# Kernel optimization log

Measured on AMD Instinct MI355X. Metric: run time of the kernel, lower is better.

## Reference

```python
import jax, jax.numpy as jnp
import numpy as np

B, S, D = 32, 512, 768
EPS = 1e-8  # torch CosineSimilarity eps

def setup_inputs() -> dict:
    key = jax.random.key(0)
    k1, k2, k3, k4 = jax.random.split(key, 4)
    emb1 = jax.random.normal(k1, (B, S, D), jnp.float32)
    emb2 = jax.random.normal(k2, (B, S, D), jnp.float32)
    mask1 = jax.random.randint(k3, (B, S), 0, 2).astype(jnp.int32)
    mask2 = jax.random.randint(k4, (B, S), 0, 2).astype(jnp.int32)
    return {"emb1": emb1, "emb2": emb2, "mask1": mask1, "mask2": mask2}

def reference(emb1, emb2, mask1, mask2):
    # normalize token embeddings (cosine sim = dot of unit vectors)
    n1 = emb1 / jnp.maximum(jnp.linalg.norm(emb1, axis=-1, keepdims=True), EPS)
    n2 = emb2 / jnp.maximum(jnp.linalg.norm(emb2, axis=-1, keepdims=True), EPS)
    # full pairwise cosine similarity: [B, S1, S2]
    sim = jnp.einsum('bid,bjd->bij', n1, n2)
    m1 = mask1.astype(sim.dtype)
    m2 = mask2.astype(sim.dtype)
    valid = m1[:, :, None] * m2[:, None, :]
    neg_inf = jnp.asarray(-jnp.inf, sim.dtype)
    masked = jnp.where(valid > 0, sim, neg_inf)
    # row max over valid cols; rows with no valid token contribute 0
    row_max = jnp.where(m1 > 0, jnp.max(masked, axis=2), 0.0)  # [B, S1]
    col_max = jnp.where(m2 > 0, jnp.max(masked, axis=1), 0.0)  # [B, S2]
    denom = jnp.sum(m1, axis=1) + jnp.sum(m2, axis=1)          # n1 + n2
    score = (jnp.sum(row_max, axis=1) + jnp.sum(col_max, axis=1)) / jnp.maximum(denom, 1.0)
    return score  # [B]
```

## Files before the change

### kernel.cpp

```cpp
#include <hip/hip_runtime.h>

#define BB 32
#define SS 512
#define DD 768

typedef float f32x4 __attribute__((ext_vector_type(4)));
typedef short bf16x8 __attribute__((ext_vector_type(8)));

__device__ __forceinline__ unsigned fkey(float f) {
  unsigned u = __float_as_uint(f);
  return (u & 0x80000000u) ? ~u : (u | 0x80000000u);
}
__device__ __forceinline__ float fdecode(unsigned k) {
  return __uint_as_float((k & 0x80000000u) ? (k & 0x7fffffffu) : ~k);
}
__device__ __forceinline__ unsigned short cvt_bf16(float f) {
  unsigned u = __float_as_uint(f);
  u += 0x7fffu + ((u >> 16) & 1u);
  return (unsigned short)(u >> 16);
}

__global__ __launch_bounds__(256) void norms_kernel(
    const float* __restrict__ emb1, const float* __restrict__ emb2,
    float* __restrict__ inv1, float* __restrict__ inv2,
    unsigned* __restrict__ rowkey, unsigned* __restrict__ colkey) {
  int wave = blockIdx.x * 4 + (threadIdx.x >> 6);
  int lane = threadIdx.x & 63;
  int half = wave >> 14;
  int r = wave & 16383;
  const float* src = (half ? emb2 : emb1) + (size_t)r * DD;
  const float4* p = (const float4*)src;
  float s = 0.f;
#pragma unroll
  for (int q = 0; q < 3; ++q) {
    float4 v = p[q * 64 + lane];
    s += v.x * v.x + v.y * v.y + v.z * v.z + v.w * v.w;
  }
#pragma unroll
  for (int m = 1; m < 64; m <<= 1) s += __shfl_xor(s, m);
  if (lane == 0) {
    float inv = 1.0f / fmaxf(sqrtf(s), 1e-8f);
    if (half == 0) { inv1[r] = inv; rowkey[r] = 0x007fffffu; }
    else           { inv2[r] = inv; colkey[r] = 0x007fffffu; }
  }
}

__global__ __launch_bounds__(256) void simmax_kernel(
    const float* __restrict__ emb1, const float* __restrict__ emb2,
    const int* __restrict__ mask1, const int* __restrict__ mask2,
    const float* __restrict__ inv1, const float* __restrict__ inv2,
    unsigned* __restrict__ rowkey, unsigned* __restrict__ colkey) {
  int b = blockIdx.y;
  int i0 = (blockIdx.x >> 2) << 7;
  int j0 = (blockIdx.x & 3) << 7;
  __shared__ __align__(16) unsigned short sA[128 * 64];
  __shared__ __align__(16) unsigned short sB[128 * 64];
  __shared__ float sInv1[128], sInv2[128];
  __shared__ int sM1[128], sM2[128];
  int t = threadIdx.x;
  if (t < 128) {
    sInv1[t] = inv1[b * SS + i0 + t];
    sM1[t]   = mask1[b * SS + i0 + t];
  } else {
    int u = t - 128;
    sInv2[u] = inv2[b * SS + j0 + u];
    sM2[u]   = mask2[b * SS + j0 + u];
  }
  const float* Ab = emb1 + ((size_t)b * SS + i0) * DD;
  const float* Bb = emb2 + ((size_t)b * SS + j0) * DD;
  int l = t & 63, wid = t >> 6, wr = wid >> 1, wc = wid & 1;
  f32x4 acc[4][4] = {};

  for (int k0 = 0; k0 < DD; k0 += 64) {
    __syncthreads();
#pragma unroll 4
    for (int pp = 0; pp < 8; ++pp) {
      int flat = pp * 256 + t;
      int r = flat >> 4, f4 = flat & 15;
      const float4 va = *(const float4*)(Ab + (size_t)r * DD + k0 + f4 * 4);
      const float4 vb = *(const float4*)(Bb + (size_t)r * DD + k0 + f4 * 4);
      int el = (r << 6) + ((((f4 >> 1) ^ (r & 7)) << 3) | ((f4 & 1) << 2));
      ushort4 ua, ub;
      ua.x = cvt_bf16(va.x); ua.y = cvt_bf16(va.y); ua.z = cvt_bf16(va.z); ua.w = cvt_bf16(va.w);
      ub.x = cvt_bf16(vb.x); ub.y = cvt_bf16(vb.y); ub.z = cvt_bf16(vb.z); ub.w = cvt_bf16(vb.w);
      *(ushort4*)(&sA[el]) = ua;
      *(ushort4*)(&sB[el]) = ub;
    }
    __syncthreads();
#pragma unroll
    for (int kk = 0; kk < 2; ++kk) {
      bf16x8 af[4], bfr[4];
#pragma unroll
      for (int mi = 0; mi < 4; ++mi) {
        int r = wr * 64 + mi * 16 + (l & 15);
        int ch = (kk << 2) + (l >> 4);
        af[mi] = *(const bf16x8*)(&sA[(r << 6) + ((ch ^ (r & 7)) << 3)]);
      }
#pragma unroll
      for (int ni = 0; ni < 4; ++ni) {
        int r = wc * 64 + ni * 16 + (l & 15);
        int ch = (kk << 2) + (l >> 4);
        bfr[ni] = *(const bf16x8*)(&sB[(r << 6) + ((ch ^ (r & 7)) << 3)]);
      }
#pragma unroll
      for (int mi = 0; mi < 4; ++mi)
#pragma unroll
        for (int ni = 0; ni < 4; ++ni)
          acc[mi][ni] = __builtin_amdgcn_mfma_f32_16x16x32_bf16(af[mi], bfr[ni], acc[mi][ni], 0, 0, 0);
    }
  }

  const float NEG = -__builtin_inff();
  float rmax[4][4], cmax[4];
#pragma unroll
  for (int mi = 0; mi < 4; ++mi)
#pragma unroll
    for (int rg = 0; rg < 4; ++rg) rmax[mi][rg] = NEG;
#pragma unroll
  for (int ni = 0; ni < 4; ++ni) cmax[ni] = NEG;

#pragma unroll
  for (int mi = 0; mi < 4; ++mi) {
#pragma unroll
    for (int ni = 0; ni < 4; ++ni) {
#pragma unroll
      for (int rg = 0; rg < 4; ++rg) {
        int rl = wr * 64 + mi * 16 + (l >> 4) * 4 + rg;
        int cl = wc * 64 + ni * 16 + (l & 15);
        float v = acc[mi][ni][rg] * sInv1[rl] * sInv2[cl];
        v = (sM1[rl] && sM2[cl]) ? v : NEG;
        rmax[mi][rg] = fmaxf(rmax[mi][rg], v);
        cmax[ni] = fmaxf(cmax[ni], v);
      }
    }
  }
#pragma unroll
  for (int mi = 0; mi < 4; ++mi)
#pragma unroll
    for (int rg = 0; rg < 4; ++rg) {
      float v = rmax[mi][rg];
      v = fmaxf(v, __shfl_xor(v, 1));
      v = fmaxf(v, __shfl_xor(v, 2));
      v = fmaxf(v, __shfl_xor(v, 4));
      v = fmaxf(v, __shfl_xor(v, 8));
      rmax[mi][rg] = v;
    }
#pragma unroll
  for (int ni = 0; ni < 4; ++ni) {
    float v = cmax[ni];
    v = fmaxf(v, __shfl_xor(v, 16));
    v = fmaxf(v, __shfl_xor(v, 32));
    cmax[ni] = v;
  }
  int selm = (l >> 2) & 3, selr = l & 3, seln = (l >> 4) & 3;
  float rv = rmax[0][0], cv = cmax[0];
#pragma unroll
  for (int mi = 0; mi < 4; ++mi)
#pragma unroll
    for (int rg = 0; rg < 4; ++rg)
      if (selm == mi && selr == rg) rv = rmax[mi][rg];
#pragma unroll
  for (int ni = 0; ni < 4; ++ni)
    if (seln == ni) cv = cmax[ni];
  int rl = selm * 16 + ((l >> 4) & 3) * 4 + selr;
  int cl = seln * 16 + (l & 15);
  atomicMax(&rowkey[b * SS + i0 + wr * 64 + rl], fkey(rv));
  atomicMax(&colkey[b * SS + j0 + wc * 64 + cl], fkey(cv));
}

__global__ __launch_bounds__(256) void finalize_kernel(
    const int* __restrict__ mask1, const int* __restrict__ mask2,
    const unsigned* __restrict__ rowkey, const unsigned* __restrict__ colkey,
    float* __restrict__ out) {
  int b = blockIdx.x, t = threadIdx.x;
  float sum = 0.f;
  int cnt = 0;
  for (int s = t; s < SS; s += 256) {
    if (mask1[b * SS + s]) { sum += fdecode(rowkey[b * SS + s]); cnt++; }
    if (mask2[b * SS + s]) { sum += fdecode(colkey[b * SS + s]); cnt++; }
  }
#pragma unroll
  for (int m = 1; m < 64; m <<= 1) {
    sum += __shfl_xor(sum, m);
    cnt += __shfl_xor(cnt, m);
  }
  __shared__ float sS[4];
  __shared__ int sC[4];
  int w = t >> 6, lane = t & 63;
  if (lane == 0) { sS[w] = sum; sC[w] = cnt; }
  __syncthreads();
  if (t == 0) {
    float T = sS[0] + sS[1] + sS[2] + sS[3];
    int C = sC[0] + sC[1] + sC[2] + sC[3];
    out[b] = T / fmaxf((float)C, 1.0f);
  }
}

extern "C" void kernel_launch(void* const* d_in, const int* in_sizes, int n_in,
                              void* d_out, int out_size, void* d_ws, size_t ws_size,
                              hipStream_t stream) {
  const float* emb1 = (const float*)d_in[0];
  const float* emb2 = (const float*)d_in[1];
  const int* mask1 = (const int*)d_in[2];
  const int* mask2 = (const int*)d_in[3];
  float* out = (float*)d_out;

  float* inv1 = (float*)d_ws;
  float* inv2 = inv1 + BB * SS;
  unsigned* rowkey = (unsigned*)(inv2 + BB * SS);
  unsigned* colkey = rowkey + BB * SS;

  norms_kernel<<<8192, 256, 0, stream>>>(emb1, emb2, inv1, inv2, rowkey, colkey);
  simmax_kernel<<<dim3(16, BB), 256, 0, stream>>>(emb1, emb2, mask1, mask2,
                                                  inv1, inv2, rowkey, colkey);
  finalize_kernel<<<BB, 256, 0, stream>>>(mask1, mask2, rowkey, colkey, out);
}
```

Baseline: 173.4 us.

## Pre-normalize to swizzled bf16 workspace and stream tiles via global_load_lds double buffering

The norm kernel now also scales each row by its inverse norm and writes it as bf16 in the swizzled shared-memory layout to a workspace. The matmul kernel then copies tiles straight into double-buffered LDS with global_load_lds, overlapping the next tile's load with MFMA work, and drops the per-element inverse-norm scaling. The 512 blocks are remapped so consecutive blocks cover different batches. This halves the bytes the matmul reads and removes in-loop conversion, at the cost of writing and rereading an extra bf16 workspace.

```diff
diff --git a/kernel.cpp b/kernel.cpp
--- a/kernel.cpp
+++ b/kernel.cpp
@@ -3,6 +3,7 @@
 #define BB 32
 #define SS 512
 #define DD 768
+#define NROW (BB * SS)
 
 typedef float f32x4 __attribute__((ext_vector_type(4)));
 typedef short bf16x8 __attribute__((ext_vector_type(8)));
@@ -20,73 +21,84 @@
   return (unsigned short)(u >> 16);
 }
 
-__global__ __launch_bounds__(256) void norms_kernel(
+__global__ __launch_bounds__(256) void norm_cvt_kernel(
     const float* __restrict__ emb1, const float* __restrict__ emb2,
-    float* __restrict__ inv1, float* __restrict__ inv2,
+    unsigned short* __restrict__ wsA, unsigned short* __restrict__ wsB,
     unsigned* __restrict__ rowkey, unsigned* __restrict__ colkey) {
   int wave = blockIdx.x * 4 + (threadIdx.x >> 6);
   int lane = threadIdx.x & 63;
   int half = wave >> 14;
-  int r = wave & 16383;
+  int r = wave & (NROW - 1);
   const float* src = (half ? emb2 : emb1) + (size_t)r * DD;
-  const float4* p = (const float4*)src;
+  float4 v[3];
   float s = 0.f;
 #pragma unroll
   for (int q = 0; q < 3; ++q) {
-    float4 v = p[q * 64 + lane];
-    s += v.x * v.x + v.y * v.y + v.z * v.z + v.w * v.w;
+    v[q] = ((const float4*)src)[q * 64 + lane];
+    s += v[q].x * v[q].x + v[q].y * v[q].y + v[q].z * v[q].z + v[q].w * v[q].w;
   }
 #pragma unroll
   for (int m = 1; m < 64; m <<= 1) s += __shfl_xor(s, m);
+  float inv = 1.0f / fmaxf(sqrtf(s), 1e-8f);
+  unsigned short* dst = (half ? wsB : wsA) + (size_t)r * DD;
+  int base = ((lane >> 4) << 6) + (((((lane >> 1) & 7) ^ (r & 7))) << 3) + ((lane & 1) << 2);
+#pragma unroll
+  for (int q = 0; q < 3; ++q) {
+    ushort4 u;
+    u.x = cvt_bf16(v[q].x * inv); u.y = cvt_bf16(v[q].y * inv);
+    u.z = cvt_bf16(v[q].z * inv); u.w = cvt_bf16(v[q].w * inv);
+    *(ushort4*)(dst + q * 256 + base) = u;
+  }
   if (lane == 0) {
-    float inv = 1.0f / fmaxf(sqrtf(s), 1e-8f);
-    if (half == 0) { inv1[r] = inv; rowkey[r] = 0x007fffffu; }
-    else           { inv2[r] = inv; colkey[r] = 0x007fffffu; }
+    if (half == 0) rowkey[r] = 0x007fffffu;
+    else           colkey[r] = 0x007fffffu;
   }
 }
 
 __global__ __launch_bounds__(256) void simmax_kernel(
-    const float* __restrict__ emb1, const float* __restrict__ emb2,
+    const unsigned short* __restrict__ wsA, const unsigned short* __restrict__ wsB,
     const int* __restrict__ mask1, const int* __restrict__ mask2,
-    const float* __restrict__ inv1, const float* __restrict__ inv2,
     unsigned* __restrict__ rowkey, unsigned* __restrict__ colkey) {
-  int b = blockIdx.y;
-  int i0 = (blockIdx.x >> 2) << 7;
-  int j0 = (blockIdx.x & 3) << 7;
-  __shared__ __align__(16) unsigned short sA[128 * 64];
-  __shared__ __align__(16) unsigned short sB[128 * 64];
-  __shared__ float sInv1[128], sInv2[128];
+  int x = blockIdx.x;
+  int b = (x & 7) + (((x >> 3) & 3) << 3);
+  int tile = x >> 5;
+  int i0 = (tile >> 2) << 7;
+  int j0 = (tile & 3) << 7;
+  __shared__ __align__(16) unsigned short sA[2][128 * 64];
+  __shared__ __align__(16) unsigned short sB[2][128 * 64];
   __shared__ int sM1[128], sM2[128];
-  int t = threadIdx.x;
-  if (t < 128) {
-    sInv1[t] = inv1[b * SS + i0 + t];
-    sM1[t]   = mask1[b * SS + i0 + t];
-  } else {
-    int u = t - 128;
-    sInv2[u] = inv2[b * SS + j0 + u];
-    sM2[u]   = mask2[b * SS + j0 + u];
-  }
-  const float* Ab = emb1 + ((size_t)b * SS + i0) * DD;
-  const float* Bb = emb2 + ((size_t)b * SS + j0) * DD;
-  int l = t & 63, wid = t >> 6, wr = wid >> 1, wc = wid & 1;
+  int t = threadIdx.x, l = t & 63, wid = t >> 6, wr = wid >> 1, wc = wid & 1;
+  if (t < 128) sM1[t] = mask1[b * SS + i0 + t];
+  else sM2[t - 128] = mask2[b * SS + j0 + (t - 128)];
+  const unsigned short* gA = wsA + (size_t)(b * SS + i0) * DD;
+  const unsigned short* gB = wsB + (size_t)(b * SS + j0) * DD;
+  int rsub = l >> 3, csub = l & 7;
+
   f32x4 acc[4][4] = {};
 
-  for (int k0 = 0; k0 < DD; k0 += 64) {
-    __syncthreads();
-#pragma unroll 4
-    for (int pp = 0; pp < 8; ++pp) {
-      int flat = pp * 256 + t;
-      int r = flat >> 4, f4 = flat & 15;
-      const float4 va = *(const float4*)(Ab + (size_t)r * DD + k0 + f4 * 4);
-      const float4 vb = *(const float4*)(Bb + (size_t)r * DD + k0 + f4 * 4);
-      int el = (r << 6) + ((((f4 >> 1) ^ (r & 7)) << 3) | ((f4 & 1) << 2));
-      ushort4 ua, ub;
-      ua.x = cvt_bf16(va.x); ua.y = cvt_bf16(va.y); ua.z = cvt_bf16(va.z); ua.w = cvt_bf16(va.w);
-      ub.x = cvt_bf16(vb.x); ub.y = cvt_bf16(vb.y); ub.z = cvt_bf16(vb.z); ub.w = cvt_bf16(vb.w);
-      *(ushort4*)(&sA[el]) = ua;
-      *(ushort4*)(&sB[el]) = ub;
-    }
-    __syncthreads();
+#define STAGE(buf, k0)                                                              \
+  {                                                                                 \
+    _Pragma("unroll") for (int j = 0; j < 4; ++j) {                                 \
+      int rowblk = (wid * 4 + j) * 8;                                               \
+      const unsigned short* ga = gA + (size_t)(rowblk + rsub) * DD + (k0) + csub * 8; \
+      const unsigned short* gb = gB + (size_t)(rowblk + rsub) * DD + (k0) + csub * 8; \
+      __builtin_amdgcn_global_load_lds(                                             \
+          (const __attribute__((address_space(1))) unsigned int*)ga,                \
+          (__attribute__((address_space(3))) unsigned int*)&sA[buf][rowblk * 64],   \
+          16, 0, 0);                                                                \
+      __builtin_amdgcn_global_load_lds(                                             \
+          (const __attribute__((address_space(1))) unsigned int*)gb,                \
+          (__attribute__((address_space(3))) unsigned int*)&sB[buf][rowblk * 64],   \
+          16, 0, 0);                                                                \
+    }                                                                               \
+  }
+
+  STAGE(0, 0);
+  __syncthreads();
+  int cur = 0;
+#pragma unroll 1
+  for (int tk = 0; tk < 12; ++tk) {
+    if (tk < 11) STAGE(cur ^ 1, (tk + 1) * 64);
 #pragma unroll
     for (int kk = 0; kk < 2; ++kk) {
       bf16x8 af[4], bfr[4];
@@ -94,13 +106,13 @@
       for (int mi = 0; mi < 4; ++mi) {
         int r = wr * 64 + mi * 16 + (l & 15);
         int ch = (kk << 2) + (l >> 4);
-        af[mi] = *(const bf16x8*)(&sA[(r << 6) + ((ch ^ (r & 7)) << 3)]);
+        af[mi] = *(const bf16x8*)(&sA[cur][(r << 6) + ((ch ^ (r & 7)) << 3)]);
       }
 #pragma unroll
       for (int ni = 0; ni < 4; ++ni) {
         int r = wc * 64 + ni * 16 + (l & 15);
         int ch = (kk << 2) + (l >> 4);
-        bfr[ni] = *(const bf16x8*)(&sB[(r << 6) + ((ch ^ (r & 7)) << 3)]);
+        bfr[ni] = *(const bf16x8*)(&sB[cur][(r << 6) + ((ch ^ (r & 7)) << 3)]);
       }
 #pragma unroll
       for (int mi = 0; mi < 4; ++mi)
@@ -108,6 +120,8 @@
         for (int ni = 0; ni < 4; ++ni)
           acc[mi][ni] = __builtin_amdgcn_mfma_f32_16x16x32_bf16(af[mi], bfr[ni], acc[mi][ni], 0, 0, 0);
     }
+    __syncthreads();
+    cur ^= 1;
   }
 
   const float NEG = -__builtin_inff();
@@ -127,7 +141,7 @@
       for (int rg = 0; rg < 4; ++rg) {
         int rl = wr * 64 + mi * 16 + (l >> 4) * 4 + rg;
         int cl = wc * 64 + ni * 16 + (l & 15);
-        float v = acc[mi][ni][rg] * sInv1[rl] * sInv2[cl];
+        float v = acc[mi][ni][rg];
         v = (sM1[rl] && sM2[cl]) ? v : NEG;
         rmax[mi][rg] = fmaxf(rmax[mi][rg], v);
         cmax[ni] = fmaxf(cmax[ni], v);
@@ -205,13 +219,12 @@
   const int* mask2 = (const int*)d_in[3];
   float* out = (float*)d_out;
 
-  float* inv1 = (float*)d_ws;
-  float* inv2 = inv1 + BB * SS;
-  unsigned* rowkey = (unsigned*)(inv2 + BB * SS);
-  unsigned* colkey = rowkey + BB * SS;
-
-  norms_kernel<<<8192, 256, 0, stream>>>(emb1, emb2, inv1, inv2, rowkey, colkey);
-  simmax_kernel<<<dim3(16, BB), 256, 0, stream>>>(emb1, emb2, mask1, mask2,
-                                                  inv1, inv2, rowkey, colkey);
+  unsigned short* wsA = (unsigned short*)d_ws;
+  unsigned short* wsB = wsA + (size_t)NROW * DD;
+  unsigned* rowkey = (unsigned*)(wsB + (size_t)NROW * DD);
+  unsigned* colkey = rowkey + NROW;
+
+  norm_cvt_kernel<<<8192, 256, 0, stream>>>(emb1, emb2, wsA, wsB, rowkey, colkey);
+  simmax_kernel<<<512, 256, 0, stream>>>(wsA, wsB, mask1, mask2, rowkey, colkey);
   finalize_kernel<<<BB, 256, 0, stream>>>(mask1, mask2, rowkey, colkey, out);
 }
```

Measured after the change: 151.2 us. -12.8%, faster.
